# Kernel tuning notes

Measured on AMD Instinct MI355X. Metric: run time of the kernel, lower is better.

The kernel has to match this reference:

```python
import jax, jax.numpy as jnp
import numpy as np

D = 512      # hidden_size
H = 8        # num_heads
DK = D // H  # head dim
B, T = 8, 1024
EPS = 1e-5


def setup_inputs() -> dict:
    key = jax.random.key(0)
    ks = jax.random.split(key, 12)
    s = 0.02
    return {
        "x": jax.random.normal(ks[0], (B, T, D), jnp.float32),
        "xlens": jax.random.randint(ks[1], (B,), 1, T + 1, jnp.int32),
        "pos_emb": jax.random.normal(ks[2], (1, 2 * T - 1, D), jnp.float32),
        "ln_gamma": jnp.ones((D,), jnp.float32),
        "ln_beta": jnp.zeros((D,), jnp.float32),
        "Wq": jax.random.normal(ks[3], (D, D), jnp.float32) * s,
        "bq": jnp.zeros((D,), jnp.float32),
        "Wk": jax.random.normal(ks[4], (D, D), jnp.float32) * s,
        "bk": jnp.zeros((D,), jnp.float32),
        "Wv": jax.random.normal(ks[5], (D, D), jnp.float32) * s,
        "bv": jnp.zeros((D,), jnp.float32),
        "Wpos": jax.random.normal(ks[6], (D, D), jnp.float32) * s,  # no bias
        "pos_bias_u": jax.random.normal(ks[7], (H, DK), jnp.float32) * s,
        "pos_bias_v": jax.random.normal(ks[8], (H, DK), jnp.float32) * s,
        "Wo": jax.random.normal(ks[9], (D, D), jnp.float32) * s,
        "bo": jnp.zeros((D,), jnp.float32),
    }


def _rel_shift(x):
    # Transformer-XL shift trick: (B, H, T, 2T-1) -> (B, H, T, T)
    b, h, t, n = x.shape
    x = jnp.pad(x, ((0, 0), (0, 0), (0, 0), (1, 0)))       # (b,h,t,2t)
    x = x.reshape(b, h, n + 1, t)[:, :, 1:, :].reshape(b, h, t, n)
    return x[..., :t]


def reference(x, xlens, pos_emb, ln_gamma, ln_beta, Wq, bq, Wk, bk, Wv, bv,
              Wpos, pos_bias_u, pos_bias_v, Wo, bo):
    b, t, d = x.shape
    # LayerNorm
    mu = jnp.mean(x, axis=-1, keepdims=True)
    var = jnp.mean(jnp.square(x - mu), axis=-1, keepdims=True)
    xn = (x - mu) * jax.lax.rsqrt(var + EPS) * ln_gamma + ln_beta

    # key padding mask: True where index >= len (padded)
    pad_mask = jnp.arange(t)[None, :] >= xlens[:, None]      # (B, T)

    q = (xn @ Wq + bq).reshape(b, t, H, DK)                  # (B,T,H,DK)
    k = (xn @ Wk + bk).reshape(b, t, H, DK)
    v = (xn @ Wv + bv).reshape(b, t, H, DK)
    p = (pos_emb @ Wpos).reshape(-1, H, DK)                  # (2T-1,H,DK)

    q_u = q + pos_bias_u                                     # (B,T,H,DK)
    q_v = q + pos_bias_v

    # content score + positional score (Transformer-XL)
    matrix_ac = jnp.einsum('bthd,bshd->bhts', q_u, k)        # (B,H,T,T)
    matrix_bd = jnp.einsum('bthd,nhd->bhtn', q_v, p)         # (B,H,T,2T-1)
    matrix_bd = _rel_shift(matrix_bd)                        # (B,H,T,T)

    scores = (matrix_ac + matrix_bd) / jnp.sqrt(jnp.float32(DK))
    scores = jnp.where(pad_mask[:, None, None, :], jnp.float32(-1e9), scores)
    attn = jax.nn.softmax(scores, axis=-1)
    attn = jnp.where(pad_mask[:, None, None, :], 0.0, attn)
    # dropout prob applied only in training; eval mode -> identity

    out = jnp.einsum('bhts,bshd->bthd', attn, v).reshape(b, t, d)
    out = out @ Wo + bo
    return out, xlens
```

## Files before the change

### kernel.cpp

```cpp
#include <hip/hip_runtime.h>
#include <stdint.h>


typedef __attribute__((ext_vector_type(8))) short s8v;
typedef __attribute__((ext_vector_type(4))) short s4v;
typedef __attribute__((ext_vector_type(4))) float f4v;
typedef unsigned short u16;

#define MFMA(a, b, c) __builtin_amdgcn_mfma_f32_16x16x32_bf16((a), (b), (c), 0, 0, 0)

__device__ __forceinline__ float bf2f(u16 u) {
    union { unsigned i; float f; } w; w.i = ((unsigned)u) << 16; return w.f;
}
__device__ __forceinline__ u16 f2bf(float f) {
    union { float f; unsigned i; } w; w.f = f;
    return (u16)((w.i + 0x7FFFu + ((w.i >> 16) & 1u)) >> 16);
}
__device__ __forceinline__ u16 f2bt(float f) {
    union { float f; unsigned i; } w; w.f = f;
    return (u16)(w.i >> 16);
}
__device__ __forceinline__ float i2f(int i) { union { int i; float f; } u; u.i = i; return u.f; }
__device__ __forceinline__ int f2i(float f) { union { float f; int i; } u; u.f = f; return u.i; }
__device__ __forceinline__ void gld16(const void* g, void* l) {
    __builtin_amdgcn_global_load_lds(
        (const __attribute__((address_space(1))) unsigned int*)g,
        (__attribute__((address_space(3))) unsigned int*)l, 16, 0, 0);
}

__global__ __launch_bounds__(256) void prep_k(
    const float* __restrict__ Wq, const float* __restrict__ Wk, const float* __restrict__ Wv,
    const float* __restrict__ Wpos, const float* __restrict__ Wo,
    const float* __restrict__ pos_emb, const int* __restrict__ xlens,
    const float* __restrict__ x, const float* __restrict__ gamma,
    const float* __restrict__ beta,
    u16* __restrict__ wt, u16* __restrict__ pe, float* __restrict__ tail,
    u16* __restrict__ xn)
{
    int bid = blockIdx.x, tid = threadIdx.x;
    if (bid < 1280) {
        __shared__ float lt[32][33];
        int mat = bid >> 8, tile = bid & 255;
        int kt = (tile >> 4) << 5, nt = (tile & 15) << 5;
        const float* W = mat == 0 ? Wq : mat == 1 ? Wk : mat == 2 ? Wv : mat == 3 ? Wpos : Wo;
        int ty = tid >> 3, tx = tid & 7;
        float4 vv = *(const float4*)&W[(kt + ty) * 512 + nt + tx * 4];
        lt[ty][tx * 4 + 0] = vv.x; lt[ty][tx * 4 + 1] = vv.y;
        lt[ty][tx * 4 + 2] = vv.z; lt[ty][tx * 4 + 3] = vv.w;
        __syncthreads();
        int nl = tid >> 3, k4 = (tid & 7) * 4;
        union { s4v v; u16 u[4]; } ob;
        #pragma unroll
        for (int e = 0; e < 4; ++e) ob.u[e] = f2bf(lt[k4 + e][nl]);
        *(s4v*)&wt[mat * 262144 + (nt + nl) * 512 + kt + k4] = ob.v;
    } else if (bid < 2304) {
        int i = (bid - 1280) * 1024 + tid * 4;
        union { s4v v; u16 u[4]; } ob;
        if (i < 2047 * 512) {
            float4 vv = *(const float4*)&pos_emb[i];
            ob.u[0] = f2bf(vv.x); ob.u[1] = f2bf(vv.y);
            ob.u[2] = f2bf(vv.z); ob.u[3] = f2bf(vv.w);
        } else {
            ob.u[0] = ob.u[1] = ob.u[2] = ob.u[3] = 0;
        }
        *(s4v*)&pe[i] = ob.v;
    } else if (bid == 2304) {
        if (tid < 8) tail[tid] = (float)xlens[tid];
    } else {
        int tok = (bid - 2305) * 4 + (tid >> 6);
        int l = tid & 63;
        const float* xr = x + (size_t)tok * 512 + l * 8;
        float v[8];
        {
            float4 a = *(const float4*)xr; float4 b = *(const float4*)(xr + 4);
            v[0] = a.x; v[1] = a.y; v[2] = a.z; v[3] = a.w;
            v[4] = b.x; v[5] = b.y; v[6] = b.z; v[7] = b.w;
        }
        float s = 0.f, q = 0.f;
        #pragma unroll
        for (int e = 0; e < 8; ++e) { s += v[e]; q += v[e] * v[e]; }
        #pragma unroll
        for (int off = 1; off < 64; off <<= 1) { s += __shfl_xor(s, off); q += __shfl_xor(q, off); }
        float mean = s * (1.f / 512.f);
        float var = q * (1.f / 512.f) - mean * mean;
        float inv = rsqrtf(var + 1e-5f);
        union { s8v v; u16 u[8]; } ob;
        #pragma unroll
        for (int e = 0; e < 8; ++e)
            ob.u[e] = f2bf((v[e] - mean) * inv * gamma[l * 8 + e] + beta[l * 8 + e]);
        *(s8v*)&xn[(size_t)tok * 512 + l * 8] = ob.v;
    }
}

__global__ __launch_bounds__(256, 2) void gemm_k(
    const u16* __restrict__ A, const u16* __restrict__ Ap, const u16* __restrict__ wt,
    const float* __restrict__ bq, const float* __restrict__ bk, const float* __restrict__ bv,
    int mode, u16* __restrict__ qo, u16* __restrict__ ko, u16* __restrict__ vtg,
    u16* __restrict__ pb, float* __restrict__ of)
{
    __shared__ u16 Al[2][128 * 64];
    __shared__ u16 Bl[2][128 * 64];
    int tid = threadIdx.x, l = tid & 63, wid = tid >> 6;
    int wr = wid >> 1, wc = wid & 1, r = l & 15, g = l >> 4;
    int m0, nb, mat;
    const u16 *Ag, *Wg;
    if (mode == 0) {
        if (blockIdx.y < 12) {
            m0 = blockIdx.x << 7; int n0 = blockIdx.y << 7;
            mat = n0 >> 9; nb = n0 & 511; Ag = A; Wg = wt + mat * 262144;
        } else {
            mat = 3; m0 = (blockIdx.x & 15) << 7; nb = (blockIdx.x >> 4) << 7;
            Ag = Ap; Wg = wt + 3 * 262144;
        }
    } else {
        mat = 4; m0 = blockIdx.x << 7; nb = blockIdx.y << 7; Ag = A; Wg = wt + 4 * 262144;
    }

    int rw8 = l >> 3;
    int csw = ((l & 7) ^ rw8) << 3;
    int off0 = ((g ^ (r & 7)) << 3);
    int off1 = (((4 + g) ^ (r & 7)) << 3);

    f4v zero = {0.f, 0.f, 0.f, 0.f};
    f4v acc[4][4];
    #pragma unroll
    for (int i = 0; i < 4; ++i)
        #pragma unroll
        for (int j = 0; j < 4; ++j) acc[i][j] = zero;

    #pragma unroll
    for (int it = 0; it < 4; ++it) {
        int rowb = wid * 32 + it * 8;
        gld16(&Ag[(size_t)(m0 + rowb + rw8) * 512 + csw], &Al[0][rowb * 64]);
        gld16(&Wg[(size_t)(nb + rowb + rw8) * 512 + csw], &Bl[0][rowb * 64]);
    }
    __syncthreads();

    for (int t = 0; t < 8; ++t) {
        int cur = t & 1;
        if (t < 7) {
            int k1 = (t + 1) << 6;
            #pragma unroll
            for (int it = 0; it < 4; ++it) {
                int rowb = wid * 32 + it * 8;
                gld16(&Ag[(size_t)(m0 + rowb + rw8) * 512 + k1 + csw], &Al[cur ^ 1][rowb * 64]);
                gld16(&Wg[(size_t)(nb + rowb + rw8) * 512 + k1 + csw], &Bl[cur ^ 1][rowb * 64]);
            }
        }
        s8v af[4][2], bfv[4][2];
        #pragma unroll
        for (int i = 0; i < 4; ++i) {
            int row = (wr * 64 + i * 16 + r) * 64;
            af[i][0] = *(const s8v*)&Al[cur][row + off0];
            af[i][1] = *(const s8v*)&Al[cur][row + off1];
        }
        #pragma unroll
        for (int j = 0; j < 4; ++j) {
            int row = (wc * 64 + j * 16 + r) * 64;
            bfv[j][0] = *(const s8v*)&Bl[cur][row + off0];
            bfv[j][1] = *(const s8v*)&Bl[cur][row + off1];
        }
        __builtin_amdgcn_s_setprio(1);
        #pragma unroll
        for (int i = 0; i < 4; ++i)
            #pragma unroll
            for (int j = 0; j < 4; ++j) {
                acc[i][j] = MFMA(af[i][0], bfv[j][0], acc[i][j]);
                acc[i][j] = MFMA(af[i][1], bfv[j][1], acc[i][j]);
            }
        __builtin_amdgcn_s_setprio(0);
        __syncthreads();
    }

    #pragma unroll
    for (int i = 0; i < 4; ++i)
        #pragma unroll
        for (int j = 0; j < 4; ++j) {
            int ncol = nb + wc * 64 + j * 16 + r;
            int mbase = m0 + wr * 64 + i * 16 + g * 4;
            if (mode == 2) {
                float bb = bq[ncol];
                #pragma unroll
                for (int jj = 0; jj < 4; ++jj)
                    of[(size_t)(mbase + jj) * 512 + ncol] = acc[i][j][jj] + bb;
            } else if (mat == 3) {
                int hh = ncol >> 6, dk = ncol & 63;
                #pragma unroll
                for (int jj = 0; jj < 4; ++jj) {
                    int m = mbase + jj;
                    if (m < 2047) pb[(hh * 2047 + m) * 64 + dk] = f2bf(acc[i][j][jj]);
                }
            } else if (mat == 2) {
                float bb = bv[ncol];
                int hh = ncol >> 6, dk = ncol & 63;
                int bbx = mbase >> 10, t = mbase & 1023;
                union { s4v v; u16 u[4]; } pk;
                #pragma unroll
                for (int jj = 0; jj < 4; ++jj) pk.u[jj] = f2bf(acc[i][j][jj] + bb);
                *(s4v*)&vtg[((size_t)(bbx * 8 + hh) * 64 + dk) * 1024 + t] = pk.v;
            } else {
                float bb = (mat == 0 ? bq : bk)[ncol];
                u16* dst = (mat == 0) ? qo : ko;
                int hh = ncol >> 6, dk = ncol & 63;
                #pragma unroll
                for (int jj = 0; jj < 4; ++jj) {
                    int m = mbase + jj;
                    int bbx = m >> 10, t = m & 1023;
                    dst[((size_t)(bbx * 8 + hh) * 1024 + t) * 64 + dk] = f2bf(acc[i][j][jj] + bb);
                }
            }
        }
}

__global__ __launch_bounds__(256, 2) void attn_k(
    const u16* __restrict__ q, const u16* __restrict__ k, const u16* __restrict__ vtg,
    const u16* __restrict__ p, const float* __restrict__ pbu, const float* __restrict__ pbv,
    const int* __restrict__ xlens, u16* __restrict__ ao)
{
    __shared__ u16 Ks[2][64 * 64];
    __shared__ u16 Vt[64 * 64];
    __shared__ u16 Ps[256 * 64];
    __shared__ u16 Tb[4][32 * 72];

    int tid = threadIdx.x, l = tid & 63, wid = tid >> 6;
    int r = l & 15, g = l >> 4, kq = g << 3;
    int t0 = blockIdx.x << 7;
    int bh = blockIdx.y, b = bh & 7, h = bh >> 3;
    int xlen = xlens[b];
    const u16* qh = q + (size_t)(b * 8 + h) * 65536;
    const u16* kh = k + (size_t)(b * 8 + h) * 65536;
    const u16* vh = vtg + (size_t)(b * 8 + h) * 65536;
    const u16* ph = p + (size_t)h * 2047 * 64;

    int rw8 = l >> 3;
    int csw = ((l & 7) ^ rw8) << 3;
    int off0 = ((g ^ (r & 7)) << 3);
    int off1 = (((4 + g) ^ (r & 7)) << 3);

    const float SCALE = 0.18033688f;

    s8v qu[2][2], qv2[2][2];
    #pragma unroll
    for (int rg = 0; rg < 2; ++rg)
        #pragma unroll
        for (int ks = 0; ks < 2; ++ks) {
            union { s8v v; u16 u[8]; } src, du, dv;
            src.v = *(const s8v*)&qh[(t0 + wid * 32 + rg * 16 + r) * 64 + ks * 32 + kq];
            float4 u0 = *(const float4*)&pbu[h * 64 + ks * 32 + kq];
            float4 u1 = *(const float4*)&pbu[h * 64 + ks * 32 + kq + 4];
            float4 v0 = *(const float4*)&pbv[h * 64 + ks * 32 + kq];
            float4 v1 = *(const float4*)&pbv[h * 64 + ks * 32 + kq + 4];
            float ub[8] = {u0.x, u0.y, u0.z, u0.w, u1.x, u1.y, u1.z, u1.w};
            float vb_[8] = {v0.x, v0.y, v0.z, v0.w, v1.x, v1.y, v1.z, v1.w};
            #pragma unroll
            for (int e = 0; e < 8; ++e) {
                float qf = bf2f(src.u[e]);
                du.u[e] = f2bf((qf + ub[e]) * SCALE);
                dv.u[e] = f2bf((qf + vb_[e]) * SCALE);
            }
            qu[rg][ks] = du.v; qv2[rg][ks] = dv.v;
        }

    int B0 = 896 - t0;
    int nst = (xlen + 63) >> 6;

    #pragma unroll
    for (int it = 0; it < 2; ++it) {
        int rowb = wid * 16 + it * 8;
        gld16(&kh[(rowb + rw8) * 64 + csw], &Ks[0][rowb * 64]);
        gld16(&vh[(rowb + rw8) * 1024 + csw], &Vt[rowb * 64]);
    }
    #pragma unroll
    for (int it = 0; it < 6; ++it) {
        int row = wid * 48 + it * 8;
        int slot = (B0 + row) & 255;
        gld16(&ph[(size_t)(B0 + row + rw8) * 64 + csw], &Ps[slot * 64]);
    }
    __syncthreads();

    float lst[2][4] = {{0.f, 0.f, 0.f, 0.f}, {0.f, 0.f, 0.f, 0.f}};
    f4v zero = {0.f, 0.f, 0.f, 0.f};
    f4v o[2][4];
    #pragma unroll
    for (int rg = 0; rg < 2; ++rg)
        #pragma unroll
        for (int i2 = 0; i2 < 4; ++i2) o[rg][i2] = zero;
    u16* tb = &Tb[wid][0];

    for (int i = 0; i < nst; ++i) {
        int cur = i & 1, s0 = i << 6;
        if (i > 0) {
            #pragma unroll
            for (int it = 0; it < 2; ++it) {
                int rowb = wid * 16 + it * 8;
                gld16(&vh[(rowb + rw8) * 1024 + s0 + csw], &Vt[rowb * 64]);
            }
        }
        if (i + 1 < nst) {
            int s1 = s0 + 64;
            #pragma unroll
            for (int it = 0; it < 2; ++it) {
                int rowb = wid * 16 + it * 8;
                gld16(&kh[(s1 + rowb + rw8) * 64 + csw], &Ks[cur ^ 1][rowb * 64]);
            }
            int base = B0 + 192 + s0;
            #pragma unroll
            for (int it = 0; it < 2; ++it) {
                int chunk = base + wid * 16 + it * 8;
                int slot = chunk & 255;
                int gp = chunk + rw8; gp = gp > 2046 ? 2046 : gp;
                gld16(&ph[(size_t)gp * 64 + csw], &Ps[slot * 64]);
            }
        }
        const u16* KB = &Ks[cur][0];
        f4v st4[2][4];
        __builtin_amdgcn_s_setprio(1);
        #pragma unroll
        for (int nf = 0; nf < 4; ++nf) {
            int row = (nf * 16 + r) * 64;
            s8v k0 = *(const s8v*)&KB[row + off0];
            s8v k1 = *(const s8v*)&KB[row + off1];
            st4[0][nf] = MFMA(qu[0][1], k1, MFMA(qu[0][0], k0, zero));
            st4[1][nf] = MFMA(qu[1][1], k1, MFMA(qu[1][0], k0, zero));
        }
        __builtin_amdgcn_s_setprio(0);
        bool full = (s0 + 64 <= xlen);
        #pragma unroll
        for (int rg = 0; rg < 2; ++rg) {
            int tbase = t0 + wid * 32 + rg * 16;
            int pstart = 1008 + s0 - tbase;
            f4v bst[5];
            __builtin_amdgcn_s_setprio(1);
            #pragma unroll
            for (int pf = 0; pf < 5; ++pf) {
                int slot = (pstart + pf * 16 + r) & 255;
                const u16* rowp = &Ps[slot * 64];
                f4v a = MFMA(qv2[rg][0], *(const s8v*)&rowp[off0], zero);
                bst[pf] = MFMA(qv2[rg][1], *(const s8v*)&rowp[off1], a);
            }
            __builtin_amdgcn_s_setprio(0);
            float pr[4][4];
            #pragma unroll
            for (int j = 0; j < 4; ++j) {
                int tl = g * 4 + j;
                int d = r + 15 - tl;
                int al = ((g << 4) | (d & 15)) << 2;
                bool lo = d < 16;
                #pragma unroll
                for (int nf = 0; nf < 4; ++nf) {
                    int xv = __builtin_amdgcn_ds_bpermute(al, f2i(bst[nf][j]));
                    int yv = __builtin_amdgcn_ds_bpermute(al, f2i(bst[nf + 1][j]));
                    float bd = i2f(lo ? xv : yv);
                    float e = exp2f(st4[rg][nf][j] + bd);
                    if (!full) e = (s0 + nf * 16 + r >= xlen) ? 0.f : e;
                    pr[nf][j] = e;
                }
            }
            #pragma unroll
            for (int j = 0; j < 4; ++j)
                lst[rg][j] += (pr[0][j] + pr[1][j]) + (pr[2][j] + pr[3][j]);
            #pragma unroll
            for (int nf = 0; nf < 4; ++nf)
                #pragma unroll
                for (int j = 0; j < 4; ++j)
                    tb[(rg * 16 + g * 4 + j) * 72 + nf * 16 + r] = f2bt(pr[nf][j]);
        }
        asm volatile("s_waitcnt lgkmcnt(0)" ::: "memory");
        __builtin_amdgcn_sched_barrier(0);
        s8v pa[2][2];
        #pragma unroll
        for (int rg = 0; rg < 2; ++rg)
            #pragma unroll
            for (int ks = 0; ks < 2; ++ks)
                pa[rg][ks] = *(const s8v*)&tb[(rg * 16 + r) * 72 + ks * 32 + kq];
        if (i > 0) {
            if (i + 1 < nst) asm volatile("s_waitcnt vmcnt(4)" ::: "memory");
            else             asm volatile("s_waitcnt vmcnt(0)" ::: "memory");
        }
        __builtin_amdgcn_s_setprio(1);
        #pragma unroll
        for (int i2 = 0; i2 < 4; ++i2) {
            int vrow = (i2 * 16 + r) * 64;
            s8v v0 = *(const s8v*)&Vt[vrow + off0];
            s8v v1 = *(const s8v*)&Vt[vrow + off1];
            o[0][i2] = MFMA(pa[0][0], v0, o[0][i2]);
            o[0][i2] = MFMA(pa[0][1], v1, o[0][i2]);
            o[1][i2] = MFMA(pa[1][0], v0, o[1][i2]);
            o[1][i2] = MFMA(pa[1][1], v1, o[1][i2]);
        }
        __builtin_amdgcn_s_setprio(0);
        __syncthreads();
    }
    #pragma unroll
    for (int rg = 0; rg < 2; ++rg)
        #pragma unroll
        for (int j = 0; j < 4; ++j) {
            float rs = lst[rg][j];
            rs += __shfl_xor(rs, 1); rs += __shfl_xor(rs, 2);
            rs += __shfl_xor(rs, 4); rs += __shfl_xor(rs, 8);
            float inv = 1.f / rs;
            int t = t0 + wid * 32 + rg * 16 + g * 4 + j;
            #pragma unroll
            for (int i2 = 0; i2 < 4; ++i2)
                ao[((size_t)(b * 1024 + t)) * 512 + h * 64 + i2 * 16 + r] =
                    f2bf(o[rg][i2][j] * inv);
        }
}

extern "C" void kernel_launch(void* const* d_in, const int* in_sizes, int n_in,
                              void* d_out, int out_size, void* d_ws, size_t ws_size,
                              hipStream_t stream)
{
    (void)in_sizes; (void)n_in; (void)out_size; (void)ws_size;
    const float* x     = (const float*)d_in[0];
    const int*   xlens = (const int*)d_in[1];
    const float* pos_e = (const float*)d_in[2];
    const float* gam   = (const float*)d_in[3];
    const float* bet   = (const float*)d_in[4];
    const float* Wq    = (const float*)d_in[5];
    const float* bq    = (const float*)d_in[6];
    const float* Wk    = (const float*)d_in[7];
    const float* bk    = (const float*)d_in[8];
    const float* Wv    = (const float*)d_in[9];
    const float* bv    = (const float*)d_in[10];
    const float* Wpos  = (const float*)d_in[11];
    const float* pbu   = (const float*)d_in[12];
    const float* pbv   = (const float*)d_in[13];
    const float* Wo    = (const float*)d_in[14];
    const float* bo    = (const float*)d_in[15];
    float* out = (float*)d_out;

    char* ws = (char*)d_ws;
    u16* xn  = (u16*)(ws);
    u16* qb  = (u16*)(ws + 8388608);
    u16* kb  = (u16*)(ws + 16777216);
    u16* vtg = (u16*)(ws + 25165824);
    u16* pbf = (u16*)(ws + 33554432);
    u16* pe  = (u16*)(ws + 35651584);
    u16* wt  = (u16*)(ws + 37748736);

    prep_k<<<4353, 256, 0, stream>>>(Wq, Wk, Wv, Wpos, Wo, pos_e, xlens,
                                     x, gam, bet, wt, pe,
                                     out + (size_t)8192 * 512, xn);
    gemm_k<<<dim3(64, 13), 256, 0, stream>>>(xn, pe, wt, bq, bk, bv, 0,
                                             qb, kb, vtg, pbf, nullptr);
    attn_k<<<dim3(8, 64), 256, 0, stream>>>(qb, kb, vtg, pbf, pbu, pbv, xlens, xn);
    gemm_k<<<dim3(64, 4), 256, 0, stream>>>(xn, nullptr, wt, bo, nullptr, nullptr, 2,
                                            nullptr, nullptr, nullptr, nullptr, out);
}
```

Measured before the change: 107.6 us.

## Load K, V and positional rows directly from global memory in attention kernel

The attention kernel drops its LDS staging of K, V^T and the positional-embedding ring buffer, along with the async copies and block barriers. Each wave now reads its MFMA operands straight from global memory, and each wave handles 16 query rows instead of 32. The grid doubles and the launch bound is raised to 4 blocks per CU. This aims to remove LDS traffic and synchronisation and to raise occupancy, at the cost of more redundant global/L2 reads, since K and V are no longer shared across waves, and less latency hiding from prefetch.

```diff
diff --git a/kernel.cpp b/kernel.cpp
--- a/kernel.cpp
+++ b/kernel.cpp
@@ -212,199 +212,134 @@
         }
 }
 
-__global__ __launch_bounds__(256, 2) void attn_k(
+__global__ __launch_bounds__(256, 4) void attn_k(
     const u16* __restrict__ q, const u16* __restrict__ k, const u16* __restrict__ vtg,
     const u16* __restrict__ p, const float* __restrict__ pbu, const float* __restrict__ pbv,
     const int* __restrict__ xlens, u16* __restrict__ ao)
 {
-    __shared__ u16 Ks[2][64 * 64];
-    __shared__ u16 Vt[64 * 64];
-    __shared__ u16 Ps[256 * 64];
-    __shared__ u16 Tb[4][32 * 72];
+    __shared__ u16 Tb[4][16 * 72];
 
     int tid = threadIdx.x, l = tid & 63, wid = tid >> 6;
     int r = l & 15, g = l >> 4, kq = g << 3;
-    int t0 = blockIdx.x << 7;
     int bh = blockIdx.y, b = bh & 7, h = bh >> 3;
+    int tw = (blockIdx.x << 6) + wid * 16;
     int xlen = xlens[b];
     const u16* qh = q + (size_t)(b * 8 + h) * 65536;
     const u16* kh = k + (size_t)(b * 8 + h) * 65536;
     const u16* vh = vtg + (size_t)(b * 8 + h) * 65536;
     const u16* ph = p + (size_t)h * 2047 * 64;
 
-    int rw8 = l >> 3;
-    int csw = ((l & 7) ^ rw8) << 3;
-    int off0 = ((g ^ (r & 7)) << 3);
-    int off1 = (((4 + g) ^ (r & 7)) << 3);
-
     const float SCALE = 0.18033688f;
 
-    s8v qu[2][2], qv2[2][2];
-    #pragma unroll
-    for (int rg = 0; rg < 2; ++rg)
-        #pragma unroll
-        for (int ks = 0; ks < 2; ++ks) {
-            union { s8v v; u16 u[8]; } src, du, dv;
-            src.v = *(const s8v*)&qh[(t0 + wid * 32 + rg * 16 + r) * 64 + ks * 32 + kq];
-            float4 u0 = *(const float4*)&pbu[h * 64 + ks * 32 + kq];
-            float4 u1 = *(const float4*)&pbu[h * 64 + ks * 32 + kq + 4];
-            float4 v0 = *(const float4*)&pbv[h * 64 + ks * 32 + kq];
-            float4 v1 = *(const float4*)&pbv[h * 64 + ks * 32 + kq + 4];
-            float ub[8] = {u0.x, u0.y, u0.z, u0.w, u1.x, u1.y, u1.z, u1.w};
-            float vb_[8] = {v0.x, v0.y, v0.z, v0.w, v1.x, v1.y, v1.z, v1.w};
-            #pragma unroll
-            for (int e = 0; e < 8; ++e) {
-                float qf = bf2f(src.u[e]);
-                du.u[e] = f2bf((qf + ub[e]) * SCALE);
-                dv.u[e] = f2bf((qf + vb_[e]) * SCALE);
+    s8v qu[2], qv[2];
+    #pragma unroll
+    for (int ks = 0; ks < 2; ++ks) {
+        union { s8v v; u16 u[8]; } src, du, dv;
+        src.v = *(const s8v*)&qh[(tw + r) * 64 + ks * 32 + kq];
+        float4 u0 = *(const float4*)&pbu[h * 64 + ks * 32 + kq];
+        float4 u1 = *(const float4*)&pbu[h * 64 + ks * 32 + kq + 4];
+        float4 v0 = *(const float4*)&pbv[h * 64 + ks * 32 + kq];
+        float4 v1 = *(const float4*)&pbv[h * 64 + ks * 32 + kq + 4];
+        float ub[8] = {u0.x, u0.y, u0.z, u0.w, u1.x, u1.y, u1.z, u1.w};
+        float vb_[8] = {v0.x, v0.y, v0.z, v0.w, v1.x, v1.y, v1.z, v1.w};
+        #pragma unroll
+        for (int e = 0; e < 8; ++e) {
+            float qf = bf2f(src.u[e]);
+            du.u[e] = f2bf((qf + ub[e]) * SCALE);
+            dv.u[e] = f2bf((qf + vb_[e]) * SCALE);
+        }
+        qu[ks] = du.v; qv[ks] = dv.v;
+    }
+
+    float lst[4] = {0.f, 0.f, 0.f, 0.f};
+    f4v zero = {0.f, 0.f, 0.f, 0.f};
+    f4v o[4] = {zero, zero, zero, zero};
+    u16* tb = &Tb[wid][0];
+    int nst = (xlen + 63) >> 6;
+
+    for (int i = 0; i < nst; ++i) {
+        int s0 = i << 6;
+        bool full = (s0 + 64 <= xlen);
+        s8v kf[4][2];
+        #pragma unroll
+        for (int nf = 0; nf < 4; ++nf) {
+            kf[nf][0] = *(const s8v*)&kh[(s0 + nf * 16 + r) * 64 + kq];
+            kf[nf][1] = *(const s8v*)&kh[(s0 + nf * 16 + r) * 64 + 32 + kq];
+        }
+        f4v st4[4];
+        __builtin_amdgcn_s_setprio(1);
+        #pragma unroll
+        for (int nf = 0; nf < 4; ++nf)
+            st4[nf] = MFMA(qu[1], kf[nf][1], MFMA(qu[0], kf[nf][0], zero));
+        __builtin_amdgcn_s_setprio(0);
+        int pstart = 1008 + s0 - tw;
+        f4v bst[5];
+        __builtin_amdgcn_s_setprio(1);
+        #pragma unroll
+        for (int pf = 0; pf < 5; ++pf) {
+            int row = pstart + pf * 16 + r; row = row > 2046 ? 2046 : row;
+            const u16* rowp = &ph[(size_t)row * 64];
+            f4v a = MFMA(qv[0], *(const s8v*)&rowp[kq], zero);
+            bst[pf] = MFMA(qv[1], *(const s8v*)&rowp[32 + kq], a);
+        }
+        __builtin_amdgcn_s_setprio(0);
+        float pr[4][4];
+        #pragma unroll
+        for (int j = 0; j < 4; ++j) {
+            int tl = g * 4 + j;
+            int d = r + 15 - tl;
+            int al = ((g << 4) | (d & 15)) << 2;
+            float bp[5];
+            #pragma unroll
+            for (int nf = 0; nf < 5; ++nf)
+                bp[nf] = i2f(__builtin_amdgcn_ds_bpermute(al, f2i(bst[nf][j])));
+            bool lo = d < 16;
+            #pragma unroll
+            for (int nf = 0; nf < 4; ++nf) {
+                float bd = lo ? bp[nf] : bp[nf + 1];
+                float e = exp2f(st4[nf][j] + bd);
+                if (!full) e = (s0 + nf * 16 + r >= xlen) ? 0.f : e;
+                pr[nf][j] = e;
             }
-            qu[rg][ks] = du.v; qv2[rg][ks] = dv.v;
-        }
-
-    int B0 = 896 - t0;
-    int nst = (xlen + 63) >> 6;
-
-    #pragma unroll
-    for (int it = 0; it < 2; ++it) {
-        int rowb = wid * 16 + it * 8;
-        gld16(&kh[(rowb + rw8) * 64 + csw], &Ks[0][rowb * 64]);
-        gld16(&vh[(rowb + rw8) * 1024 + csw], &Vt[rowb * 64]);
-    }
-    #pragma unroll
-    for (int it = 0; it < 6; ++it) {
-        int row = wid * 48 + it * 8;
-        int slot = (B0 + row) & 255;
-        gld16(&ph[(size_t)(B0 + row + rw8) * 64 + csw], &Ps[slot * 64]);
-    }
-    __syncthreads();
-
-    float lst[2][4] = {{0.f, 0.f, 0.f, 0.f}, {0.f, 0.f, 0.f, 0.f}};
-    f4v zero = {0.f, 0.f, 0.f, 0.f};
-    f4v o[2][4];
-    #pragma unroll
-    for (int rg = 0; rg < 2; ++rg)
-        #pragma unroll
-        for (int i2 = 0; i2 < 4; ++i2) o[rg][i2] = zero;
-    u16* tb = &Tb[wid][0];
-
-    for (int i = 0; i < nst; ++i) {
-        int cur = i & 1, s0 = i << 6;
-        if (i > 0) {
-            #pragma unroll
-            for (int it = 0; it < 2; ++it) {
-                int rowb = wid * 16 + it * 8;
-                gld16(&vh[(rowb + rw8) * 1024 + s0 + csw], &Vt[rowb * 64]);
-            }
-        }
-        if (i + 1 < nst) {
-            int s1 = s0 + 64;
-            #pragma unroll
-            for (int it = 0; it < 2; ++it) {
-                int rowb = wid * 16 + it * 8;
-                gld16(&kh[(s1 + rowb + rw8) * 64 + csw], &Ks[cur ^ 1][rowb * 64]);
-            }
-            int base = B0 + 192 + s0;
-            #pragma unroll
-            for (int it = 0; it < 2; ++it) {
-                int chunk = base + wid * 16 + it * 8;
-                int slot = chunk & 255;
-                int gp = chunk + rw8; gp = gp > 2046 ? 2046 : gp;
-                gld16(&ph[(size_t)gp * 64 + csw], &Ps[slot * 64]);
-            }
-        }
-        const u16* KB = &Ks[cur][0];
-        f4v st4[2][4];
-        __builtin_amdgcn_s_setprio(1);
-        #pragma unroll
-        for (int nf = 0; nf < 4; ++nf) {
-            int row = (nf * 16 + r) * 64;
-            s8v k0 = *(const s8v*)&KB[row + off0];
-            s8v k1 = *(const s8v*)&KB[row + off1];
-            st4[0][nf] = MFMA(qu[0][1], k1, MFMA(qu[0][0], k0, zero));
-            st4[1][nf] = MFMA(qu[1][1], k1, MFMA(qu[1][0], k0, zero));
-        }
-        __builtin_amdgcn_s_setprio(0);
-        bool full = (s0 + 64 <= xlen);
-        #pragma unroll
-        for (int rg = 0; rg < 2; ++rg) {
-            int tbase = t0 + wid * 32 + rg * 16;
-            int pstart = 1008 + s0 - tbase;
-            f4v bst[5];
-            __builtin_amdgcn_s_setprio(1);
-            #pragma unroll
-            for (int pf = 0; pf < 5; ++pf) {
-                int slot = (pstart + pf * 16 + r) & 255;
-                const u16* rowp = &Ps[slot * 64];
-                f4v a = MFMA(qv2[rg][0], *(const s8v*)&rowp[off0], zero);
-                bst[pf] = MFMA(qv2[rg][1], *(const s8v*)&rowp[off1], a);
-            }
-            __builtin_amdgcn_s_setprio(0);
-            float pr[4][4];
-            #pragma unroll
-            for (int j = 0; j < 4; ++j) {
-                int tl = g * 4 + j;
-                int d = r + 15 - tl;
-                int al = ((g << 4) | (d & 15)) << 2;
-                bool lo = d < 16;
-                #pragma unroll
-                for (int nf = 0; nf < 4; ++nf) {
-                    int xv = __builtin_amdgcn_ds_bpermute(al, f2i(bst[nf][j]));
-                    int yv = __builtin_amdgcn_ds_bpermute(al, f2i(bst[nf + 1][j]));
-                    float bd = i2f(lo ? xv : yv);
-                    float e = exp2f(st4[rg][nf][j] + bd);
-                    if (!full) e = (s0 + nf * 16 + r >= xlen) ? 0.f : e;
-                    pr[nf][j] = e;
-                }
-            }
+        }
+        #pragma unroll
+        for (int j = 0; j < 4; ++j)
+            lst[j] += (pr[0][j] + pr[1][j]) + (pr[2][j] + pr[3][j]);
+        #pragma unroll
+        for (int nf = 0; nf < 4; ++nf)
             #pragma unroll
             for (int j = 0; j < 4; ++j)
-                lst[rg][j] += (pr[0][j] + pr[1][j]) + (pr[2][j] + pr[3][j]);
-            #pragma unroll
-            for (int nf = 0; nf < 4; ++nf)
-                #pragma unroll
-                for (int j = 0; j < 4; ++j)
-                    tb[(rg * 16 + g * 4 + j) * 72 + nf * 16 + r] = f2bt(pr[nf][j]);
-        }
+                tb[(g * 4 + j) * 72 + nf * 16 + r] = f2bt(pr[nf][j]);
         asm volatile("s_waitcnt lgkmcnt(0)" ::: "memory");
         __builtin_amdgcn_sched_barrier(0);
-        s8v pa[2][2];
-        #pragma unroll
-        for (int rg = 0; rg < 2; ++rg)
-            #pragma unroll
-            for (int ks = 0; ks < 2; ++ks)
-                pa[rg][ks] = *(const s8v*)&tb[(rg * 16 + r) * 72 + ks * 32 + kq];
-        if (i > 0) {
-            if (i + 1 < nst) asm volatile("s_waitcnt vmcnt(4)" ::: "memory");
-            else             asm volatile("s_waitcnt vmcnt(0)" ::: "memory");
+        s8v pa0 = *(const s8v*)&tb[r * 72 + kq];
+        s8v pa1 = *(const s8v*)&tb[r * 72 + 32 + kq];
+        s8v vf[4][2];
+        #pragma unroll
+        for (int i2 = 0; i2 < 4; ++i2) {
+            const u16* vrow = &vh[(size_t)(i2 * 16 + r) * 1024 + s0];
+            vf[i2][0] = *(const s8v*)&vrow[kq];
+            vf[i2][1] = *(const s8v*)&vrow[32 + kq];
         }
         __builtin_amdgcn_s_setprio(1);
         #pragma unroll
         for (int i2 = 0; i2 < 4; ++i2) {
-            int vrow = (i2 * 16 + r) * 64;
-            s8v v0 = *(const s8v*)&Vt[vrow + off0];
-            s8v v1 = *(const s8v*)&Vt[vrow + off1];
-            o[0][i2] = MFMA(pa[0][0], v0, o[0][i2]);
-            o[0][i2] = MFMA(pa[0][1], v1, o[0][i2]);
-            o[1][i2] = MFMA(pa[1][0], v0, o[1][i2]);
-            o[1][i2] = MFMA(pa[1][1], v1, o[1][i2]);
+            o[i2] = MFMA(pa0, vf[i2][0], o[i2]);
+            o[i2] = MFMA(pa1, vf[i2][1], o[i2]);
         }
         __builtin_amdgcn_s_setprio(0);
-        __syncthreads();
-    }
-    #pragma unroll
-    for (int rg = 0; rg < 2; ++rg)
-        #pragma unroll
-        for (int j = 0; j < 4; ++j) {
-            float rs = lst[rg][j];
-            rs += __shfl_xor(rs, 1); rs += __shfl_xor(rs, 2);
-            rs += __shfl_xor(rs, 4); rs += __shfl_xor(rs, 8);
-            float inv = 1.f / rs;
-            int t = t0 + wid * 32 + rg * 16 + g * 4 + j;
-            #pragma unroll
-            for (int i2 = 0; i2 < 4; ++i2)
-                ao[((size_t)(b * 1024 + t)) * 512 + h * 64 + i2 * 16 + r] =
-                    f2bf(o[rg][i2][j] * inv);
-        }
+    }
+    #pragma unroll
+    for (int j = 0; j < 4; ++j) {
+        float rs = lst[j];
+        rs += __shfl_xor(rs, 1); rs += __shfl_xor(rs, 2);
+        rs += __shfl_xor(rs, 4); rs += __shfl_xor(rs, 8);
+        float inv = 1.f / rs;
+        int t = tw + g * 4 + j;
+        #pragma unroll
+        for (int i2 = 0; i2 < 4; ++i2)
+            ao[((size_t)(b * 1024 + t)) * 512 + h * 64 + i2 * 16 + r] = f2bf(o[i2][j] * inv);
+    }
 }
 
 extern "C" void kernel_launch(void* const* d_in, const int* in_sizes, int n_in,
@@ -444,7 +379,7 @@
                                      out + (size_t)8192 * 512, xn);
     gemm_k<<<dim3(64, 13), 256, 0, stream>>>(xn, pe, wt, bq, bk, bv, 0,
                                              qb, kb, vtg, pbf, nullptr);
-    attn_k<<<dim3(8, 64), 256, 0, stream>>>(qb, kb, vtg, pbf, pbu, pbv, xlens, xn);
+    attn_k<<<dim3(16, 64), 256, 0, stream>>>(qb, kb, vtg, pbf, pbu, pbv, xlens, xn);
     gemm_k<<<dim3(64, 4), 256, 0, stream>>>(xn, nullptr, wt, bo, nullptr, nullptr, 2,
                                             nullptr, nullptr, nullptr, nullptr, out);
 }
```

Result: slower. 241.2 us (+124.1%).
